# Performance work log

Hardware: AMD Instinct MI355X
Metric: run time of the kernel (lower is better)

Reference implementation:

```python
import jax, jax.numpy as jnp
import numpy as np

D, FF, E, K = 1024, 1024, 8, 2  # d_model, ffn_dim, n_experts, top_k
B, S = 4, 1024


def _gelu(x):
    # torch F.gelu default is the exact erf form
    return jax.nn.gelu(x, approximate=False)


def setup_inputs() -> dict:
    key = jax.random.key(0)
    ks = jax.random.split(key, 12)
    s = 0.02
    return {
        "x": jax.random.normal(ks[0], (B, S, D), jnp.float32),
        "gate_w": jax.random.normal(ks[1], (D, E), jnp.float32) * s,
        "gate_b": jnp.zeros((E,), jnp.float32),
        # shared expert (n_shared = 1)
        "sw1": jax.random.normal(ks[2], (D, FF), jnp.float32) * s,
        "sb1": jnp.zeros((FF,), jnp.float32),
        "sw2": jax.random.normal(ks[3], (FF, D), jnp.float32) * s,
        "sb2": jnp.zeros((D,), jnp.float32),
        # routed experts, stacked over E
        "w1": jax.random.normal(ks[4], (E, D, FF), jnp.float32) * s,
        "b1": jnp.zeros((E, FF), jnp.float32),
        "w2": jax.random.normal(ks[5], (E, FF, D), jnp.float32) * s,
        "b2": jnp.zeros((E, D), jnp.float32),
    }


def reference(x, gate_w, gate_b, sw1, sb1, sw2, sb2, w1, b1, w2, b2):
    Bb, Ss, Dm = x.shape
    t = x.reshape(-1, Dm)  # [T, D]
    T = t.shape[0]

    # shared expert(s)
    shared = _gelu(t @ sw1 + sb1) @ sw2 + sb2  # [T, D]

    # gating: softmax over experts, then top-k
    probs = jax.nn.softmax(t @ gate_w + gate_b, axis=-1)  # [T, E]
    topk_p, topk_i = jax.lax.top_k(probs, K)  # [T, K]

    # combine weights: sparse [T, E] with top-k probs (top_k indices are distinct)
    combine = jnp.zeros((T, E), t.dtype).at[
        jnp.arange(T)[:, None], topk_i
    ].set(topk_p)

    # expert FFNs computed densely, combined with sparse routing weights;
    # mathematically identical to the masked gather-GEMM-scatter loop
    h = _gelu(jnp.einsum("td,edf->etf", t, w1) + b1[:, None, :])  # [E, T, FF]
    y = jnp.einsum("etf,efd->etd", h, w2) + b2[:, None, :]        # [E, T, D]
    routed = jnp.einsum("te,etd->td", combine, y)                  # [T, D]

    return (routed + shared).reshape(Bb, Ss, Dm)
```

## Files before the change

kernel.cpp:

```cpp
#include <hip/hip_runtime.h>
#include <hip/hip_bf16.h>


typedef short short8 __attribute__((ext_vector_type(8)));
typedef float f32x4  __attribute__((ext_vector_type(4)));

#define T_TOK 4096
#define NSLOT 8192

#define OFF_XB    (size_t)0
#define OFF_W1T   (size_t)8388608
#define OFF_W2T   (size_t)25165824
#define OFF_SW1T  (size_t)41943040
#define OFF_SW2T  (size_t)44040192
#define OFF_HS    (size_t)46137344
#define OFF_HR    (size_t)54525952
#define OFF_META  (size_t)73400320
#define OFF_ROWMAP (size_t)73400576
#define OFF_ROWW  (size_t)73437440
#define OFF_TKI   (size_t)73474304
#define OFF_TKP   (size_t)73507072

__device__ __forceinline__ unsigned short f2bf(float f) {
  __hip_bfloat16 h = __float2bfloat16(f);
  return __builtin_bit_cast(unsigned short, h);
}
__device__ __forceinline__ float gelu_exact(float x) {
  return 0.5f * x * (1.0f + erff(x * 0.70710678118654752f));
}

#define GLOAD16(g, l)                                                          \
  __builtin_amdgcn_global_load_lds(                                            \
      (const __attribute__((address_space(1))) void*)(g),                      \
      (__attribute__((address_space(3))) void*)(l), 16, 0, 0)


__global__ void k_transpose(const float* __restrict__ w1, const float* __restrict__ w2,
                            const float* __restrict__ sw1, const float* __restrict__ sw2,
                            unsigned short* __restrict__ w1t, unsigned short* __restrict__ w2t,
                            unsigned short* __restrict__ sw1t, unsigned short* __restrict__ sw2t) {
  __shared__ float tile[32][33];
  int z = blockIdx.z;
  const float* src; unsigned short* dst;
  if (z < 8)       { src = w1 + (size_t)z * 1048576;        dst = w1t + (size_t)z * 1048576; }
  else if (z < 16) { src = w2 + (size_t)(z - 8) * 1048576;  dst = w2t + (size_t)(z - 8) * 1048576; }
  else if (z == 16){ src = sw1; dst = sw1t; }
  else             { src = sw2; dst = sw2t; }
  int tx = threadIdx.x, ty = threadIdx.y;
  int gx = blockIdx.x * 32 + tx;
#pragma unroll
  for (int j = 0; j < 4; j++) {
    int gy = blockIdx.y * 32 + ty + j * 8;
    tile[ty + j * 8][tx] = src[(size_t)gy * 1024 + gx];
  }
  __syncthreads();
#pragma unroll
  for (int j = 0; j < 4; j++) {
    int orow = blockIdx.x * 32 + ty + j * 8;
    int ocol = blockIdx.y * 32 + tx;
    dst[(size_t)orow * 1024 + ocol] = f2bf(tile[tx][ty + j * 8]);
  }
}

__global__ void k_convert_x(const float* __restrict__ x, unsigned short* __restrict__ xb) {
  int i = blockIdx.x * blockDim.x + threadIdx.x;
  float4 v = ((const float4*)x)[i];
  ushort4 o;
  o.x = f2bf(v.x); o.y = f2bf(v.y); o.z = f2bf(v.z); o.w = f2bf(v.w);
  ((ushort4*)xb)[i] = o;
}

__global__ void k_gate(const float* __restrict__ x, const float* __restrict__ gw,
                       const float* __restrict__ gb, int* __restrict__ tki,
                       float* __restrict__ tkp) {
  int wv = threadIdx.x >> 6, l = threadIdx.x & 63;
  int t = blockIdx.x * 4 + wv;
  float acc[8] = {0, 0, 0, 0, 0, 0, 0, 0};
  const float* xr = x + (size_t)t * 1024;
#pragma unroll
  for (int j = 0; j < 16; j++) {
    int k = j * 64 + l;
    float xv = xr[k];
    const float4* g4 = (const float4*)(gw + (size_t)k * 8);
    float4 ga = g4[0], gbv = g4[1];
    acc[0] += xv * ga.x; acc[1] += xv * ga.y; acc[2] += xv * ga.z; acc[3] += xv * ga.w;
    acc[4] += xv * gbv.x; acc[5] += xv * gbv.y; acc[6] += xv * gbv.z; acc[7] += xv * gbv.w;
  }
#pragma unroll
  for (int off = 32; off > 0; off >>= 1) {
#pragma unroll
    for (int e = 0; e < 8; e++) acc[e] += __shfl_xor(acc[e], off);
  }
  if (l == 0) {
    float lg[8], p[8];
    float m = -1e30f;
#pragma unroll
    for (int e = 0; e < 8; e++) { lg[e] = acc[e] + gb[e]; m = fmaxf(m, lg[e]); }
    float s = 0.f;
#pragma unroll
    for (int e = 0; e < 8; e++) { p[e] = expf(lg[e] - m); s += p[e]; }
    float inv = 1.0f / s;
#pragma unroll
    for (int e = 0; e < 8; e++) p[e] *= inv;
    int i0 = 0;
#pragma unroll
    for (int e = 1; e < 8; e++) if (p[e] > p[i0]) i0 = e;
    int i1 = (i0 == 0) ? 1 : 0;
#pragma unroll
    for (int e = 0; e < 8; e++) if (e != i0 && p[e] > p[i1]) i1 = e;
    tki[t * 2] = i0; tki[t * 2 + 1] = i1;
    tkp[t * 2] = p[i0]; tkp[t * 2 + 1] = p[i1];
  }
}

__global__ void k_count(const int* __restrict__ tki, int* __restrict__ counts) {
  int e = blockIdx.x, tid = threadIdx.x;
  int c = 0;
  for (int i = tid; i < NSLOT; i += 256) c += (tki[i] == e);
  __shared__ int red[256];
  red[tid] = c;
  __syncthreads();
#pragma unroll
  for (int s = 128; s > 0; s >>= 1) {
    if (tid < s) red[tid] += red[tid + s];
    __syncthreads();
  }
  if (tid == 0) counts[e] = red[0];
}

__global__ void k_plan(const int* __restrict__ counts, int* __restrict__ base) {
  int off = 0;
  for (int e = 0; e < 8; e++) {
    base[e] = off;
    off += (counts[e] + 127) & ~127;
  }
}

__global__ void k_scatter(const int* __restrict__ tki, const float* __restrict__ tkp,
                          const int* __restrict__ base, int* __restrict__ rowmap,
                          float* __restrict__ roww) {
  int e = blockIdx.x, tid = threadIdx.x;
  int lane = tid & 63, wv = tid >> 6;
  __shared__ int warpsum[4];
  __shared__ int blockoff;
  if (tid == 0) blockoff = base[e];
  __syncthreads();
  for (int i0 = 0; i0 < NSLOT; i0 += 256) {
    int i = i0 + tid;
    bool pred = (tki[i] == e);
    unsigned long long mask = __ballot(pred);
    int wpre = __popcll(mask & ((1ull << lane) - 1));
    if (lane == 0) warpsum[wv] = __popcll(mask);
    __syncthreads();
    int wbase = 0;
    for (int w = 0; w < wv; w++) wbase += warpsum[w];
    int total = warpsum[0] + warpsum[1] + warpsum[2] + warpsum[3];
    int boff = blockoff;
    if (pred) {
      int pos = boff + wbase + wpre;
      rowmap[pos] = i >> 1;
      roww[pos] = tkp[i];
    }
    __syncthreads();
    if (tid == 0) blockoff = boff + total;
    __syncthreads();
  }
}

template <int MODE>
__global__ __launch_bounds__(256, 2) void k_gemm(
    const unsigned short* __restrict__ A, const unsigned short* __restrict__ Bw,
    const float* __restrict__ bias, float* __restrict__ outf,
    unsigned short* __restrict__ outh, const int* __restrict__ rowmap,
    const float* __restrict__ roww, const int* __restrict__ counts,
    const int* __restrict__ bases) {
  __shared__ unsigned short ldsA[128 * 64];
  __shared__ unsigned short ldsB[128 * 64];

  int e = (MODE == 1 || MODE == 3) ? blockIdx.z : 0;
  const unsigned short* Bmat = Bw + (size_t)e * 1048576;
  const float* bvec = bias + (size_t)e * 1024;
  int nrows = 0, rbase = 0;
  int row0 = blockIdx.y * 128;
  if (MODE == 1 || MODE == 3) {
    nrows = counts[e];
    rbase = bases[e];
    if (row0 >= nrows) return;
  }
  int n0 = blockIdx.x * 128;
  int tid = threadIdx.x, wave = tid >> 6, lane = tid & 63;
  int wm = wave >> 1, wn = wave & 1;

  f32x4 acc[4][4];
#pragma unroll
  for (int i = 0; i < 4; i++)
#pragma unroll
    for (int j = 0; j < 4; j++) acc[i][j] = (f32x4){0.f, 0.f, 0.f, 0.f};

  for (int k0 = 0; k0 < 1024; k0 += 64) {
#pragma unroll
    for (int i = 0; i < 4; i++) {
      int q = i * 4 + wave;
      int c = q * 64 + lane;
      int m = c >> 3, s = c & 7;
      int ks = s ^ (m & 7);
      long arow;
      if (MODE == 1) {
        int r = row0 + m; if (r >= nrows) r = nrows - 1;
        arow = rowmap[rbase + r];
      } else if (MODE == 3) {
        arow = rbase + row0 + m;
      } else {
        arow = row0 + m;
      }
      GLOAD16(A + arow * 1024 + k0 + ks * 8, &ldsA[q * 512]);
    }
#pragma unroll
    for (int i = 0; i < 4; i++) {
      int q = i * 4 + wave;
      int c = q * 64 + lane;
      int n = c >> 3, s = c & 7;
      int ks = s ^ (n & 7);
      GLOAD16(Bmat + (size_t)(n0 + n) * 1024 + k0 + ks * 8, &ldsB[q * 512]);
    }
    __syncthreads();
#pragma unroll
    for (int kk = 0; kk < 2; kk++) {
      short8 af[4], bfr[4];
      int kc0 = kk * 4 + (lane >> 4);
#pragma unroll
      for (int fi = 0; fi < 4; fi++) {
        int m = wm * 64 + fi * 16 + (lane & 15);
        int slot = kc0 ^ (m & 7);
        af[fi] = *(const short8*)&ldsA[m * 64 + slot * 8];
      }
#pragma unroll
      for (int fj = 0; fj < 4; fj++) {
        int n = wn * 64 + fj * 16 + (lane & 15);
        int slot = kc0 ^ (n & 7);
        bfr[fj] = *(const short8*)&ldsB[n * 64 + slot * 8];
      }
#pragma unroll
      for (int fi = 0; fi < 4; fi++)
#pragma unroll
        for (int fj = 0; fj < 4; fj++)
          acc[fi][fj] = __builtin_amdgcn_mfma_f32_16x16x32_bf16(af[fi], bfr[fj], acc[fi][fj], 0, 0, 0);
    }
    __syncthreads();
  }

#pragma unroll
  for (int fi = 0; fi < 4; fi++) {
#pragma unroll
    for (int rg = 0; rg < 4; rg++) {
      int lr = wm * 64 + fi * 16 + (lane >> 4) * 4 + rg;
      int r = row0 + lr;
      if (MODE == 3) {
        if (r < nrows) {
          int tok = rowmap[rbase + r];
          float p = roww[rbase + r];
#pragma unroll
          for (int fj = 0; fj < 4; fj++) {
            int col = n0 + wn * 64 + fj * 16 + (lane & 15);
            atomicAdd(&outf[(size_t)tok * 1024 + col], p * (acc[fi][fj][rg] + bvec[col]));
          }
        }
      } else if (MODE == 2) {
#pragma unroll
        for (int fj = 0; fj < 4; fj++) {
          int col = n0 + wn * 64 + fj * 16 + (lane & 15);
          outf[(size_t)r * 1024 + col] = acc[fi][fj][rg] + bias[col];
        }
      } else if (MODE == 1) {
#pragma unroll
        for (int fj = 0; fj < 4; fj++) {
          int col = n0 + wn * 64 + fj * 16 + (lane & 15);
          outh[(size_t)(rbase + r) * 1024 + col] = f2bf(gelu_exact(acc[fi][fj][rg] + bvec[col]));
        }
      } else {
#pragma unroll
        for (int fj = 0; fj < 4; fj++) {
          int col = n0 + wn * 64 + fj * 16 + (lane & 15);
          outh[(size_t)r * 1024 + col] = f2bf(gelu_exact(acc[fi][fj][rg] + bias[col]));
        }
      }
    }
  }
}

extern "C" void kernel_launch(void* const* d_in, const int* in_sizes, int n_in,
                              void* d_out, int out_size, void* d_ws, size_t ws_size,
                              hipStream_t stream) {
  const float* x   = (const float*)d_in[0];
  const float* gw  = (const float*)d_in[1];
  const float* gb  = (const float*)d_in[2];
  const float* sw1 = (const float*)d_in[3];
  const float* sb1 = (const float*)d_in[4];
  const float* sw2 = (const float*)d_in[5];
  const float* sb2 = (const float*)d_in[6];
  const float* w1  = (const float*)d_in[7];
  const float* b1  = (const float*)d_in[8];
  const float* w2  = (const float*)d_in[9];
  const float* b2  = (const float*)d_in[10];
  float* out = (float*)d_out;
  char* ws = (char*)d_ws;

  unsigned short* xb   = (unsigned short*)(ws + OFF_XB);
  unsigned short* w1t  = (unsigned short*)(ws + OFF_W1T);
  unsigned short* w2t  = (unsigned short*)(ws + OFF_W2T);
  unsigned short* sw1t = (unsigned short*)(ws + OFF_SW1T);
  unsigned short* sw2t = (unsigned short*)(ws + OFF_SW2T);
  unsigned short* Hs   = (unsigned short*)(ws + OFF_HS);
  unsigned short* Hr   = (unsigned short*)(ws + OFF_HR);
  int*   counts = (int*)(ws + OFF_META);
  int*   basev  = counts + 8;
  int*   rowmap = (int*)(ws + OFF_ROWMAP);
  float* roww   = (float*)(ws + OFF_ROWW);
  int*   tki    = (int*)(ws + OFF_TKI);
  float* tkp    = (float*)(ws + OFF_TKP);

  k_transpose<<<dim3(32, 32, 18), dim3(32, 8), 0, stream>>>(w1, w2, sw1, sw2, w1t, w2t, sw1t, sw2t);
  k_convert_x<<<4096, 256, 0, stream>>>(x, xb);
  k_gate<<<1024, 256, 0, stream>>>(x, gw, gb, tki, tkp);
  k_count<<<8, 256, 0, stream>>>(tki, counts);
  k_plan<<<1, 1, 0, stream>>>(counts, basev);
  k_scatter<<<8, 256, 0, stream>>>(tki, tkp, basev, rowmap, roww);

  k_gemm<0><<<dim3(8, 32), 256, 0, stream>>>(xb, sw1t, sb1, nullptr, Hs, nullptr, nullptr, nullptr, nullptr);
  k_gemm<1><<<dim3(8, 32, 8), 256, 0, stream>>>(xb, w1t, b1, nullptr, Hr, rowmap, roww, counts, basev);
  k_gemm<2><<<dim3(8, 32), 256, 0, stream>>>(Hs, sw2t, sb2, out, nullptr, nullptr, nullptr, nullptr, nullptr);
  k_gemm<3><<<dim3(8, 32, 8), 256, 0, stream>>>(Hr, w2t, b2, out, nullptr, rowmap, roww, counts, basev);
}
```

Before: 215.5 us.

## Merge shared and routed expert GEMMs into single launches with 64-row tiles

Replaces four GEMM launches with two: each phase handles the shared expert (z=0) and all routed experts (z=1..8) in one grid. The M tile shrinks from 128 to 64 rows, expert padding drops to 64, and launch bounds rise to 4 blocks per CU, so there are more blocks, better occupancy and less padded work. Gather row indices are hoisted out of the K loop. The shared second GEMM now atomically adds into an output that is explicitly zeroed first. The cost is more atomics plus a memset, and lower per-block operand reuse with the smaller tile.

```diff
diff --git a/kernel.cpp b/kernel.cpp
--- a/kernel.cpp
+++ b/kernel.cpp
@@ -132,7 +132,7 @@
   int off = 0;
   for (int e = 0; e < 8; e++) {
     base[e] = off;
-    off += (counts[e] + 127) & ~127;
+    off += (counts[e] + 63) & ~63;
   }
 }
 
@@ -167,53 +167,66 @@
   }
 }
 
-template <int MODE>
-__global__ __launch_bounds__(256, 2) void k_gemm(
-    const unsigned short* __restrict__ A, const unsigned short* __restrict__ Bw,
-    const float* __restrict__ bias, float* __restrict__ outf,
-    unsigned short* __restrict__ outh, const int* __restrict__ rowmap,
-    const float* __restrict__ roww, const int* __restrict__ counts,
-    const int* __restrict__ bases) {
-  __shared__ unsigned short ldsA[128 * 64];
+template <int PHASE>
+__global__ __launch_bounds__(256, 4) void k_ffn(
+    const unsigned short* __restrict__ As,
+    const unsigned short* __restrict__ Ar,
+    const unsigned short* __restrict__ Bsh, const float* __restrict__ bsh,
+    const unsigned short* __restrict__ Brt, const float* __restrict__ brt,
+    unsigned short* __restrict__ Hsh, unsigned short* __restrict__ Hrt,
+    float* __restrict__ outf,
+    const int* __restrict__ rowmap, const float* __restrict__ roww,
+    const int* __restrict__ counts, const int* __restrict__ bases) {
+  __shared__ unsigned short ldsA[64 * 64];
   __shared__ unsigned short ldsB[128 * 64];
 
-  int e = (MODE == 1 || MODE == 3) ? blockIdx.z : 0;
-  const unsigned short* Bmat = Bw + (size_t)e * 1048576;
-  const float* bvec = bias + (size_t)e * 1024;
-  int nrows = 0, rbase = 0;
-  int row0 = blockIdx.y * 128;
-  if (MODE == 1 || MODE == 3) {
-    nrows = counts[e];
-    rbase = bases[e];
+  int z = blockIdx.z;
+  int row0 = blockIdx.y * 64;
+  int nrows, rbase = 0;
+  const unsigned short* Bmat;
+  const float* bvec;
+  const unsigned short* Amat;
+  if (z == 0) {
+    nrows = T_TOK;
+    Bmat = Bsh; bvec = bsh; Amat = As;
+  } else {
+    int e = z - 1;
+    nrows = counts[e]; rbase = bases[e];
     if (row0 >= nrows) return;
+    Bmat = Brt + (size_t)e * 1048576;
+    bvec = brt + (size_t)e * 1024;
+    Amat = (PHASE == 1) ? As : Ar;
   }
   int n0 = blockIdx.x * 128;
   int tid = threadIdx.x, wave = tid >> 6, lane = tid & 63;
   int wm = wave >> 1, wn = wave & 1;
 
-  f32x4 acc[4][4];
-#pragma unroll
-  for (int i = 0; i < 4; i++)
+  long arow[2];
+#pragma unroll
+  for (int i = 0; i < 2; i++) {
+    int q = i * 4 + wave;
+    int m = (q * 64 + lane) >> 3;
+    int r = row0 + m;
+    if (r >= nrows) r = nrows - 1;
+    if (z == 0)            arow[i] = r;
+    else if (PHASE == 1)   arow[i] = rowmap[rbase + r];
+    else                   arow[i] = rbase + r;
+  }
+
+  f32x4 acc[2][4];
+#pragma unroll
+  for (int i = 0; i < 2; i++)
 #pragma unroll
     for (int j = 0; j < 4; j++) acc[i][j] = (f32x4){0.f, 0.f, 0.f, 0.f};
 
   for (int k0 = 0; k0 < 1024; k0 += 64) {
 #pragma unroll
-    for (int i = 0; i < 4; i++) {
+    for (int i = 0; i < 2; i++) {
       int q = i * 4 + wave;
       int c = q * 64 + lane;
       int m = c >> 3, s = c & 7;
       int ks = s ^ (m & 7);
-      long arow;
-      if (MODE == 1) {
-        int r = row0 + m; if (r >= nrows) r = nrows - 1;
-        arow = rowmap[rbase + r];
-      } else if (MODE == 3) {
-        arow = rbase + row0 + m;
-      } else {
-        arow = row0 + m;
-      }
-      GLOAD16(A + arow * 1024 + k0 + ks * 8, &ldsA[q * 512]);
+      GLOAD16(Amat + arow[i] * 1024 + k0 + ks * 8, &ldsA[q * 512]);
     }
 #pragma unroll
     for (int i = 0; i < 4; i++) {
@@ -226,11 +239,11 @@
     __syncthreads();
 #pragma unroll
     for (int kk = 0; kk < 2; kk++) {
-      short8 af[4], bfr[4];
+      short8 af[2], bfr[4];
       int kc0 = kk * 4 + (lane >> 4);
 #pragma unroll
-      for (int fi = 0; fi < 4; fi++) {
-        int m = wm * 64 + fi * 16 + (lane & 15);
+      for (int fi = 0; fi < 2; fi++) {
+        int m = wm * 32 + fi * 16 + (lane & 15);
         int slot = kc0 ^ (m & 7);
         af[fi] = *(const short8*)&ldsA[m * 64 + slot * 8];
       }
@@ -241,7 +254,7 @@
         bfr[fj] = *(const short8*)&ldsB[n * 64 + slot * 8];
       }
 #pragma unroll
-      for (int fi = 0; fi < 4; fi++)
+      for (int fi = 0; fi < 2; fi++)
 #pragma unroll
         for (int fj = 0; fj < 4; fj++)
           acc[fi][fj] = __builtin_amdgcn_mfma_f32_16x16x32_bf16(af[fi], bfr[fj], acc[fi][fj], 0, 0, 0);
@@ -250,13 +263,28 @@
   }
 
 #pragma unroll
-  for (int fi = 0; fi < 4; fi++) {
+  for (int fi = 0; fi < 2; fi++) {
 #pragma unroll
     for (int rg = 0; rg < 4; rg++) {
-      int lr = wm * 64 + fi * 16 + (lane >> 4) * 4 + rg;
+      int lr = wm * 32 + fi * 16 + (lane >> 4) * 4 + rg;
       int r = row0 + lr;
-      if (MODE == 3) {
-        if (r < nrows) {
+      if (r >= nrows) continue;
+      if (PHASE == 1) {
+        unsigned short* dst = (z == 0) ? (Hsh + (size_t)r * 1024)
+                                       : (Hrt + (size_t)(rbase + r) * 1024);
+#pragma unroll
+        for (int fj = 0; fj < 4; fj++) {
+          int col = n0 + wn * 64 + fj * 16 + (lane & 15);
+          dst[col] = f2bf(gelu_exact(acc[fi][fj][rg] + bvec[col]));
+        }
+      } else {
+        if (z == 0) {
+#pragma unroll
+          for (int fj = 0; fj < 4; fj++) {
+            int col = n0 + wn * 64 + fj * 16 + (lane & 15);
+            atomicAdd(&outf[(size_t)r * 1024 + col], acc[fi][fj][rg] + bvec[col]);
+          }
+        } else {
           int tok = rowmap[rbase + r];
           float p = roww[rbase + r];
 #pragma unroll
@@ -264,24 +292,6 @@
             int col = n0 + wn * 64 + fj * 16 + (lane & 15);
             atomicAdd(&outf[(size_t)tok * 1024 + col], p * (acc[fi][fj][rg] + bvec[col]));
           }
-        }
-      } else if (MODE == 2) {
-#pragma unroll
-        for (int fj = 0; fj < 4; fj++) {
-          int col = n0 + wn * 64 + fj * 16 + (lane & 15);
-          outf[(size_t)r * 1024 + col] = acc[fi][fj][rg] + bias[col];
-        }
-      } else if (MODE == 1) {
-#pragma unroll
-        for (int fj = 0; fj < 4; fj++) {
-          int col = n0 + wn * 64 + fj * 16 + (lane & 15);
-          outh[(size_t)(rbase + r) * 1024 + col] = f2bf(gelu_exact(acc[fi][fj][rg] + bvec[col]));
-        }
-      } else {
-#pragma unroll
-        for (int fj = 0; fj < 4; fj++) {
-          int col = n0 + wn * 64 + fj * 16 + (lane & 15);
-          outh[(size_t)r * 1024 + col] = f2bf(gelu_exact(acc[fi][fj][rg] + bias[col]));
         }
       }
     }
@@ -325,9 +335,10 @@
   k_count<<<8, 256, 0, stream>>>(tki, counts);
   k_plan<<<1, 1, 0, stream>>>(counts, basev);
   k_scatter<<<8, 256, 0, stream>>>(tki, tkp, basev, rowmap, roww);
-
-  k_gemm<0><<<dim3(8, 32), 256, 0, stream>>>(xb, sw1t, sb1, nullptr, Hs, nullptr, nullptr, nullptr, nullptr);
-  k_gemm<1><<<dim3(8, 32, 8), 256, 0, stream>>>(xb, w1t, b1, nullptr, Hr, rowmap, roww, counts, basev);
-  k_gemm<2><<<dim3(8, 32), 256, 0, stream>>>(Hs, sw2t, sb2, out, nullptr, nullptr, nullptr, nullptr, nullptr);
-  k_gemm<3><<<dim3(8, 32, 8), 256, 0, stream>>>(Hr, w2t, b2, out, nullptr, rowmap, roww, counts, basev);
-}
+  hipMemsetAsync(out, 0, (size_t)out_size * sizeof(float), stream);
+
+  k_ffn<1><<<dim3(8, 64, 9), 256, 0, stream>>>(xb, xb, sw1t, sb1, w1t, b1, Hs, Hr,
+                                               nullptr, rowmap, roww, counts, basev);
+  k_ffn<2><<<dim3(8, 64, 9), 256, 0, stream>>>(Hs, Hr, sw2t, sb2, w2t, b2, nullptr, nullptr,
+                                               out, rowmap, roww, counts, basev);
+}
```

After: 192.2 us. 10.8% less time.
